# Optimization experiments

Hardware: AMD Instinct MI355X
Metric: run time of the kernel (lower is better)

The kernel has to match this reference:

```python
import jax, jax.numpy as jnp
import numpy as np

B, S, D, H = 2, 2048, 1024, 16
HD = D // H  # 64
ROPE_BASE = 10000.0


def setup_inputs() -> dict:
    key = jax.random.key(0)
    k1, k2, k3 = jax.random.split(key, 3)
    std = 1.0 / np.sqrt(D)
    x = jax.random.normal(k1, (B, S, D), dtype=jnp.float32)
    w_in = jax.random.normal(k2, (3 * D, D), dtype=jnp.float32) * std
    w_out = jax.random.normal(k3, (D, D), dtype=jnp.float32) * (std / np.sqrt(2.0))
    return {"x": x, "w_in": w_in, "w_out": w_out}


def _rope_cos_sin(seq_len, head_dim):
    inv_freq = 1.0 / (ROPE_BASE ** (jnp.arange(0, head_dim, 2, dtype=jnp.float32) / head_dim))
    t = jnp.arange(seq_len, dtype=jnp.float32)
    freqs = jnp.einsum("s,d->sd", t, inv_freq)          # [S, HD/2]
    emb = jnp.concatenate([freqs, freqs], axis=-1)       # [S, HD]
    return jnp.cos(emb)[None, :, None, :], jnp.sin(emb)[None, :, None, :]


def _rotate_half(x):
    x1, x2 = jnp.split(x, 2, axis=-1)
    return jnp.concatenate([-x2, x1], axis=-1)


def _apply_rope(x, cos, sin):
    return x * cos + _rotate_half(x) * sin


def reference(x, w_in, w_out):
    b, s, d = x.shape
    # fused QKV projection (no bias)
    qkv = x @ w_in.T                                      # [B, S, 3D]
    q, k, v = jnp.split(qkv, 3, axis=-1)
    q = q.reshape(b, s, H, HD)
    k = k.reshape(b, s, H, HD)
    v = v.reshape(b, s, H, HD)
    # rotary (offset = 0, no KV cache)
    cos, sin = _rope_cos_sin(s, HD)
    q = _apply_rope(q, cos, sin)
    k = _apply_rope(k, cos, sin)
    # causal SDPA, scale 1/sqrt(head_dim)
    scale = 1.0 / jnp.sqrt(jnp.asarray(HD, dtype=x.dtype))
    scores = jnp.einsum("bqhd,bkhd->bhqk", q, k) * scale  # [B, H, S, S]
    causal = jnp.tril(jnp.ones((s, s), dtype=bool))
    scores = jnp.where(causal, scores, jnp.asarray(-jnp.inf, dtype=scores.dtype))
    attn = jax.nn.softmax(scores, axis=-1)
    out = jnp.einsum("bhqk,bkhd->bqhd", attn, v).reshape(b, s, d)
    return out @ w_out.T
```

## Files before the change

kernel.cpp:

```cpp
#include <hip/hip_runtime.h>
#include <hip/hip_bf16.h>
#include <math.h>

#define NB 2
#define NS 2048
#define ND 1024
#define NH 16
#define HD 64
#define BS (NB*NS)
#define D3 (3*ND)
#define NT (NS/64)

typedef __bf16 bf16;
typedef __bf16 bf16x4 __attribute__((ext_vector_type(4)));
typedef __bf16 bf16x8 __attribute__((ext_vector_type(8)));
typedef float f32x4 __attribute__((ext_vector_type(4)));

#define MFMA16(a,b,c) __builtin_amdgcn_mfma_f32_16x16x32_bf16(a,b,c,0,0,0)

static __device__ inline f32x4 zero4() { f32x4 z; z[0]=0.f; z[1]=0.f; z[2]=0.f; z[3]=0.f; return z; }

__device__ __forceinline__ void gload_lds16(const bf16* g, bf16* l) {
    __builtin_amdgcn_global_load_lds(
        (__attribute__((address_space(1))) unsigned int*)g,
        (__attribute__((address_space(3))) unsigned int*)l, 16, 0, 0);
}

#define CVT1 (BS*ND/8)
#define CVT2 (D3*ND/8)
#define CVT3 (ND*ND/8)
#define CVTN (CVT1+CVT2+CVT3)
__global__ __launch_bounds__(256) void prep(
    const float* __restrict__ x, const float* __restrict__ w_in, const float* __restrict__ w_out,
    bf16* __restrict__ xb, bf16* __restrict__ winb, bf16* __restrict__ woutb,
    float2* __restrict__ csT)
{
    int i = blockIdx.x * 256 + threadIdx.x;
    if (i < CVTN) {
        const float* in; bf16* out; int j;
        if (i < CVT1)            { in = x;     out = xb;    j = i; }
        else if (i < CVT1+CVT2)  { in = w_in;  out = winb;  j = i - CVT1; }
        else                     { in = w_out; out = woutb; j = i - CVT1 - CVT2; }
        const float4* p = (const float4*)in;
        float4 a = p[j*2], b = p[j*2+1];
        bf16x8 o;
        o[0]=(bf16)a.x; o[1]=(bf16)a.y; o[2]=(bf16)a.z; o[3]=(bf16)a.w;
        o[4]=(bf16)b.x; o[5]=(bf16)b.y; o[6]=(bf16)b.z; o[7]=(bf16)b.w;
        ((bf16x8*)out)[j] = o;
    } else {
        int k = i - CVTN;
        int s = k >> 5, j = k & 31;
        float inv = __expf(-(float)j * (9.210340372f * 0.03125f));
        float ang = (float)s * inv;
        csT[k] = make_float2(cosf(ang), sinf(ang));
    }
}

__global__ __launch_bounds__(256, 2) void gemm_qkv(
    const bf16* __restrict__ A, const bf16* __restrict__ Bm,
    bf16* __restrict__ Qb, bf16* __restrict__ Kb, bf16* __restrict__ Vt,
    const float2* __restrict__ csT)
{
    __shared__ bf16 As[2][128*64];
    __shared__ bf16 Bs[2][192*64];
    int t = threadIdx.x;
    int lane = t & 63, w = t >> 6;
    int lr = lane & 15, lg = lane >> 4;
    int m0 = blockIdx.y * 128, n0 = blockIdx.x * 192;

    int srow8 = lane >> 3;
    int schunk = (lane & 7) ^ srow8;
    const bf16* gA = A  + (size_t)(m0 + srow8)*ND + schunk*8;
    const bf16* gB = Bm + (size_t)(n0 + srow8)*ND + schunk*8;

    auto stage = [&](int kt) {
        int buf = kt & 1, k0 = kt*64;
        #pragma unroll
        for (int i=0;i<4;i++) {
            int r0 = w*32 + i*8;
            gload_lds16(gA + (size_t)r0*ND + k0, &As[buf][r0*64]);
        }
        #pragma unroll
        for (int i=0;i<6;i++) {
            int r0 = w*48 + i*8;
            gload_lds16(gB + (size_t)r0*ND + k0, &Bs[buf][r0*64]);
        }
    };

    f32x4 acc[2][12];
    #pragma unroll
    for (int mm=0;mm<2;mm++)
        #pragma unroll
        for (int n=0;n<12;n++) acc[mm][n] = zero4();

    bf16x8 af[2][2], bfr[4][2];

    stage(0); stage(1);

    for (int kt = 0; kt < 16; kt++) {
        int cur = kt & 1;
        const bf16* as = &As[cur][0];
        const bf16* bs = &Bs[cur][0];
        if (kt < 15) asm volatile("s_waitcnt vmcnt(10)" ::: "memory");
        else         asm volatile("s_waitcnt vmcnt(0)" ::: "memory");
        __builtin_amdgcn_s_barrier();
        __builtin_amdgcn_sched_barrier(0);

        #pragma unroll
        for (int mm=0;mm<2;mm++) {
            int row = w*32 + mm*16 + lr;
            af[mm][0] = *(const bf16x8*)&as[row*64 + ((lg     ^ (row&7))*8)];
            af[mm][1] = *(const bf16x8*)&as[row*64 + (((4+lg) ^ (row&7))*8)];
        }

        #pragma unroll
        for (int g=0; g<3; g++) {
            #pragma unroll
            for (int nn=0;nn<4;nn++) {
                int row = g*64 + nn*16 + lr;
                bfr[nn][0] = *(const bf16x8*)&bs[row*64 + ((lg     ^ (row&7))*8)];
                bfr[nn][1] = *(const bf16x8*)&bs[row*64 + (((4+lg) ^ (row&7))*8)];
            }
            asm volatile("s_waitcnt lgkmcnt(0)" ::: "memory");
            __builtin_amdgcn_sched_barrier(0);
            if (g == 2) {
                __builtin_amdgcn_s_barrier();
                __builtin_amdgcn_sched_barrier(0);
                if (kt + 2 < 16) stage(kt + 2);
            }
            __builtin_amdgcn_s_setprio(1);
            #pragma unroll
            for (int ks=0;ks<2;ks++)
                #pragma unroll
                for (int mm=0;mm<2;mm++)
                    #pragma unroll
                    for (int nn=0;nn<4;nn++)
                        acc[mm][g*4+nn] = MFMA16(af[mm][ks], bfr[nn][ks], acc[mm][g*4+nn]);
            __builtin_amdgcn_s_setprio(0);
        }
    }

    const float qs = 0.125f * 1.44269504f;
    #pragma unroll
    for (int a=0;a<3;a++) {
        int colbase = n0 + a*64;
        int which = colbase >> 10;
        if (which == 2) {
            #pragma unroll
            for (int p=0;p<4;p++)
                #pragma unroll
                for (int mm=0;mm<2;mm++) {
                    int gcol = colbase + p*16 + lr;
                    int h = (gcol & 1023) >> 6, d = gcol & 63;
                    int grow = m0 + w*32 + mm*16 + lg*4;
                    int b = grow >> 11, s0 = grow & (NS-1);
                    int shi = s0 & ~63, j = s0 & 63;
                    int kp = ((j>>5)&1)*32 + ((j>>2)&3)*8 + ((j>>4)&1)*4;
                    bf16x4 pv;
                    #pragma unroll
                    for (int r=0;r<4;r++) pv[r] = (bf16)acc[mm][a*4+p][r];
                    *(bf16x4*)&Vt[((size_t)((b*NH + h)*HD + d))*NS + shi + kp] = pv;
                }
        } else {
            bf16* dst = (which == 0) ? Qb : Kb;
            #pragma unroll
            for (int p=0;p<2;p++)
                #pragma unroll
                for (int mm=0;mm<2;mm++) {
                    int gcol = colbase + p*16 + lr;
                    int h = (gcol & 1023) >> 6, j = gcol & 63;
                    int grow = m0 + w*32 + mm*16 + lg*4;
                    #pragma unroll
                    for (int r=0;r<4;r++) {
                        int gm = grow + r;
                        int b = gm >> 11, s = gm & (NS-1);
                        float2 cs = csT[(s<<5)+j];
                        float x1 = acc[mm][a*4+p][r], x2 = acc[mm][a*4+p+2][r];
                        float y1 = x1*cs.x - x2*cs.y;
                        float y2 = x2*cs.x + x1*cs.y;
                        if (which == 0) { y1 *= qs; y2 *= qs; }
                        size_t off = ((size_t)((b*NH + h)*NS + s))*HD;
                        dst[off + j]      = (bf16)y1;
                        dst[off + j + 32] = (bf16)y2;
                    }
                }
        }
    }
}

__global__ __launch_bounds__(256) void gemm_out(
    const bf16* __restrict__ A, const bf16* __restrict__ Bm,
    float* __restrict__ C, int M, int N, int K)
{
    __shared__ bf16 As[2][128*64];
    __shared__ bf16 Bs[2][128*64];
    int t = threadIdx.x;
    int lane = t & 63, w = t >> 6;
    int wr = w >> 1, wc = w & 1;
    int lr = lane & 15, lg = lane >> 4;
    int m0 = blockIdx.y * 128, n0 = blockIdx.x * 128;

    int srow = lane >> 3;
    int schunk = (lane & 7) ^ srow;
    const bf16* gA = &A [(size_t)(m0 + w*32 + srow)*K + schunk*8];
    const bf16* gB = &Bm[(size_t)(n0 + w*32 + srow)*K + schunk*8];

    auto stage = [&](int kt) {
        int buf = kt & 1;
        bf16* lA = &As[buf][w*2048];
        bf16* lB = &Bs[buf][w*2048];
        int k0 = kt * 64;
        #pragma unroll
        for (int i=0;i<4;i++) {
            gload_lds16(gA + (size_t)(i*8)*K + k0, lA + i*512);
            gload_lds16(gB + (size_t)(i*8)*K + k0, lB + i*512);
        }
    };

    f32x4 acc[4][4];
    for (int m=0;m<4;m++) for (int n=0;n<4;n++) acc[m][n] = zero4();

    int nt = K >> 6;
    stage(0);
    stage(1);

    for (int kt = 0; kt < nt; kt++) {
        int cur = kt & 1;
        if (kt < nt-1) asm volatile("s_waitcnt vmcnt(8)" ::: "memory");
        else           asm volatile("s_waitcnt vmcnt(0)" ::: "memory");
        __builtin_amdgcn_s_barrier();
        __builtin_amdgcn_sched_barrier(0);

        bf16x8 af[2][4], bfr[2][4];
        #pragma unroll
        for (int ks=0;ks<2;ks++) {
            #pragma unroll
            for (int m=0;m<4;m++) {
                int row = wr*64 + m*16 + lr;
                af[ks][m] = *(const bf16x8*)&As[cur][row*64 + (((ks*4+lg) ^ (row&7))*8)];
            }
            #pragma unroll
            for (int n=0;n<4;n++) {
                int row = wc*64 + n*16 + lr;
                bfr[ks][n] = *(const bf16x8*)&Bs[cur][row*64 + (((ks*4+lg) ^ (row&7))*8)];
            }
        }
        asm volatile("s_waitcnt lgkmcnt(0)" ::: "memory");
        __builtin_amdgcn_sched_barrier(0);
        __builtin_amdgcn_s_barrier();
        __builtin_amdgcn_sched_barrier(0);

        if (kt + 2 < nt) stage(kt + 2);

        __builtin_amdgcn_s_setprio(1);
        #pragma unroll
        for (int ks=0;ks<2;ks++)
            #pragma unroll
            for (int m=0;m<4;m++)
                #pragma unroll
                for (int n=0;n<4;n++)
                    acc[m][n] = MFMA16(af[ks][m], bfr[ks][n], acc[m][n]);
        __builtin_amdgcn_s_setprio(0);
    }

    for (int m=0;m<4;m++) for (int n=0;n<4;n++) {
        int grow = m0 + wr*64 + m*16 + lg*4;
        int gcol = n0 + wc*64 + n*16 + lr;
        for (int r=0;r<4;r++)
            C[(size_t)(grow+r) * N + gcol] = acc[m][n][r];
    }
}

__global__ __launch_bounds__(256, 4) void attn_fwd(
    const bf16* __restrict__ Qb, const bf16* __restrict__ Kb, const bf16* __restrict__ Vp,
    bf16* __restrict__ AO)
{
    __shared__ bf16 Ks[2][64*64];
    __shared__ bf16 Vs[2][64*64];
    int t = threadIdx.x;
    int lane = t & 63, w = t >> 6;
    int lr = lane & 15, lg = lane >> 4;
    int wgid = blockIdx.x;
    int g = wgid >> 5;
    int qt = (g < 8) ? 31 - g : (g < 16) ? g - 8 : (g < 24) ? 39 - g : g - 16;
    int bh = wgid & 31;
    int b = bh >> 4, h = bh & 15;
    size_t base = (size_t)bh * NS * HD;
    int q0 = qt*64 + w*16;

    bf16x8 qf[2];
    #pragma unroll
    for (int c=0;c<2;c++)
        qf[c] = *(const bf16x8*)&Qb[base + (size_t)(q0+lr)*HD + c*32 + lg*8];

    bf16x8 onesf;
    #pragma unroll
    for (int i=0;i<8;i++) onesf[i] = (bf16)1.0f;

    f32x4 o[4];
    f32x4 lacc = zero4();
    #pragma unroll
    for (int n=0;n<4;n++) o[n] = zero4();
    f32x4 minit;
    minit[0] = -12.f; minit[1] = -12.f; minit[2] = -12.f; minit[3] = -12.f;

    int srow8 = lane >> 3;
    int schunk = (lane & 7) ^ srow8;
    int srcrow = w*8 + srow8;
    const bf16* gK = Kb + base + (size_t)srcrow*HD + schunk*8;
    const bf16* gV = Vp + base + (size_t)srcrow*NS + schunk*8;

    auto stage = [&](int kt) {
        int buf = kt & 1;
        int kv0 = kt * 64;
        #pragma unroll
        for (int i=0;i<2;i++) {
            gload_lds16(gK + (size_t)(kv0 + i*32)*HD, &Ks[buf][(i*32 + w*8)*64]);
            gload_lds16(gV + (size_t)(i*32)*NS + kv0, &Vs[buf][(i*32 + w*8)*64]);
        }
    };

    stage(0);
    if (qt > 0) stage(1);

    for (int kt = 0; kt <= qt; kt++) {
        int cur = kt & 1;
        bool last = (kt == qt);
        if (!last) asm volatile("s_waitcnt vmcnt(4)" ::: "memory");
        else       asm volatile("s_waitcnt vmcnt(0)" ::: "memory");
        __builtin_amdgcn_s_barrier();
        __builtin_amdgcn_sched_barrier(0);

        const bf16* ksb = &Ks[cur][0];
        const bf16* vsb = &Vs[cur][0];

        bf16x8 kf[4][2], vf[2][4];
        #pragma unroll
        for (int kb=0;kb<4;kb++) {
            int row = kb*16 + lr;
            kf[kb][0] = *(const bf16x8*)&ksb[row*64 + ((lg     ^ (row&7))*8)];
            kf[kb][1] = *(const bf16x8*)&ksb[row*64 + (((4+lg) ^ (row&7))*8)];
        }
        #pragma unroll
        for (int c=0;c<2;c++)
            #pragma unroll
            for (int n=0;n<4;n++) {
                int row = n*16 + lr;
                vf[c][n] = *(const bf16x8*)&vsb[row*64 + (((c*4+lg) ^ (row&7))*8)];
            }

        f32x4 sc[4];
        __builtin_amdgcn_s_setprio(1);
        #pragma unroll
        for (int kb=0;kb<4;kb++) {
            sc[kb] = MFMA16(kf[kb][0], qf[0], minit);
            sc[kb] = MFMA16(kf[kb][1], qf[1], sc[kb]);
        }
        __builtin_amdgcn_s_setprio(0);

        if (last) {
            int qi = q0 + lr;
            #pragma unroll
            for (int kb=0;kb<4;kb++)
                #pragma unroll
                for (int rr=0;rr<4;rr++)
                    if (kt*64 + kb*16 + lg*4 + rr > qi) sc[kb][rr] = -__builtin_inff();
        }

        bf16x8 pa[2];
        #pragma unroll
        for (int c=0;c<2;c++) {
            bf16x8 v;
            #pragma unroll
            for (int i=0;i<8;i++) v[i] = (bf16)exp2f(sc[c*2 + (i>>2)][i&3]);
            pa[c] = v;
        }

        asm volatile("s_waitcnt lgkmcnt(0)" ::: "memory");
        __builtin_amdgcn_sched_barrier(0);
        __builtin_amdgcn_s_barrier();
        __builtin_amdgcn_sched_barrier(0);

        if (kt + 2 <= qt) stage(kt + 2);

        __builtin_amdgcn_s_setprio(1);
        #pragma unroll
        for (int c=0;c<2;c++) {
            lacc = MFMA16(onesf, pa[c], lacc);
            #pragma unroll
            for (int n=0;n<4;n++)
                o[n] = MFMA16(vf[c][n], pa[c], o[n]);
        }
        __builtin_amdgcn_s_setprio(0);
    }

    float inv = 1.0f / lacc[0];
    int q = q0 + lr;
    #pragma unroll
    for (int n=0;n<4;n++) {
        bf16x4 ov;
        #pragma unroll
        for (int rr=0;rr<4;rr++) ov[rr] = (bf16)(o[n][rr] * inv);
        *(bf16x4*)&AO[((size_t)(b*NS + q)*NH + h)*HD + n*16 + lg*4] = ov;
    }
}

extern "C" void kernel_launch(void* const* d_in, const int* in_sizes, int n_in,
                              void* d_out, int out_size, void* d_ws, size_t ws_size,
                              hipStream_t stream) {
    const float* x     = (const float*)d_in[0];
    const float* w_in  = (const float*)d_in[1];
    const float* w_out = (const float*)d_in[2];
    float* out = (float*)d_out;

    char* p = (char*)d_ws;
    bf16* xb    = (bf16*)p; p += (size_t)BS*ND*2;
    bf16* winb  = (bf16*)p; p += (size_t)D3*ND*2;
    bf16* woutb = (bf16*)p; p += (size_t)ND*ND*2;
    bf16* Qb    = (bf16*)p; p += (size_t)NB*NH*NS*HD*2;
    bf16* Kb    = (bf16*)p; p += (size_t)NB*NH*NS*HD*2;
    bf16* Vp    = (bf16*)p; p += (size_t)NB*NH*NS*HD*2;
    bf16* AO    = (bf16*)p; p += (size_t)BS*ND*2;
    float2* csT = (float2*)p; p += (size_t)NS*32*8;

    prep<<<(CVTN + NS*32)/256, 256, 0, stream>>>(x, w_in, w_out, xb, winb, woutb, csT);
    gemm_qkv<<<dim3(D3/192, BS/128), 256, 0, stream>>>(xb, winb, Qb, Kb, Vp, csT);
    attn_fwd<<<NB*NH*NT, 256, 0, stream>>>(Qb, Kb, Vp, AO);
    gemm_out<<<dim3(ND/128, BS/128), 256, 0, stream>>>(AO, woutb, out, BS, ND, ND);
}
```

Measured before the change: 91.50 us.

## Rewrite attention with 32x32x16 MFMA and 128-row query tiles

The attention kernel now uses 32x32x16 bf16 MFMAs. Each workgroup covers 128 query rows (32 per wave) instead of 64, which halves the grid and shares each staged K/V tile across more queries. The P-matrix operand layout is rebuilt with cross-half-wave shuffles, and the V transpose layout in the QKV GEMM epilogue is simplified to match. Waves skip fully masked key tiles. In exchange, register pressure rises (occupancy hint lowered to 2), shuffles are added, the grid has fewer blocks, and waves in the same block do uneven amounts of work.

```diff
diff --git a/kernel.cpp b/kernel.cpp
--- a/kernel.cpp
+++ b/kernel.cpp
@@ -15,8 +15,11 @@
 typedef __bf16 bf16x4 __attribute__((ext_vector_type(4)));
 typedef __bf16 bf16x8 __attribute__((ext_vector_type(8)));
 typedef float f32x4 __attribute__((ext_vector_type(4)));
+typedef float f32x16 __attribute__((ext_vector_type(16)));
+typedef unsigned int u32;
 
 #define MFMA16(a,b,c) __builtin_amdgcn_mfma_f32_16x16x32_bf16(a,b,c,0,0,0)
+#define MFMA32(a,b,c) __builtin_amdgcn_mfma_f32_32x32x16_bf16(a,b,c,0,0,0)
 
 static __device__ inline f32x4 zero4() { f32x4 z; z[0]=0.f; z[1]=0.f; z[2]=0.f; z[3]=0.f; return z; }
 
@@ -154,12 +157,10 @@
                     int h = (gcol & 1023) >> 6, d = gcol & 63;
                     int grow = m0 + w*32 + mm*16 + lg*4;
                     int b = grow >> 11, s0 = grow & (NS-1);
-                    int shi = s0 & ~63, j = s0 & 63;
-                    int kp = ((j>>5)&1)*32 + ((j>>2)&3)*8 + ((j>>4)&1)*4;
                     bf16x4 pv;
                     #pragma unroll
                     for (int r=0;r<4;r++) pv[r] = (bf16)acc[mm][a*4+p][r];
-                    *(bf16x4*)&Vt[((size_t)((b*NH + h)*HD + d))*NS + shi + kp] = pv;
+                    *(bf16x4*)&Vt[((size_t)((b*NH + h)*HD + d))*NS + s0] = pv;
                 }
         } else {
             bf16* dst = (which == 0) ? Qb : Kb;
@@ -271,7 +272,7 @@
     }
 }
 
-__global__ __launch_bounds__(256, 4) void attn_fwd(
+__global__ __launch_bounds__(256, 2) void attn_fwd(
     const bf16* __restrict__ Qb, const bf16* __restrict__ Kb, const bf16* __restrict__ Vp,
     bf16* __restrict__ AO)
 {
@@ -279,30 +280,29 @@
     __shared__ bf16 Vs[2][64*64];
     int t = threadIdx.x;
     int lane = t & 63, w = t >> 6;
-    int lr = lane & 15, lg = lane >> 4;
+    int lq = lane & 31, hh = lane >> 5;
     int wgid = blockIdx.x;
     int g = wgid >> 5;
-    int qt = (g < 8) ? 31 - g : (g < 16) ? g - 8 : (g < 24) ? 39 - g : g - 16;
+    int qt2 = (g < 8) ? 15 - g : g - 8;
     int bh = wgid & 31;
     int b = bh >> 4, h = bh & 15;
     size_t base = (size_t)bh * NS * HD;
-    int q0 = qt*64 + w*16;
-
-    bf16x8 qf[2];
-    #pragma unroll
-    for (int c=0;c<2;c++)
-        qf[c] = *(const bf16x8*)&Qb[base + (size_t)(q0+lr)*HD + c*32 + lg*8];
+    int q0w = qt2*128 + w*32;
+    int q = q0w + lq;
+    int nvis = 2*qt2 + 2;
+
+    bf16x8 qf[4];
+    #pragma unroll
+    for (int tt=0;tt<4;tt++)
+        qf[tt] = *(const bf16x8*)&Qb[base + (size_t)q*HD + tt*16 + hh*8];
 
     bf16x8 onesf;
     #pragma unroll
     for (int i=0;i<8;i++) onesf[i] = (bf16)1.0f;
 
-    f32x4 o[4];
-    f32x4 lacc = zero4();
-    #pragma unroll
-    for (int n=0;n<4;n++) o[n] = zero4();
-    f32x4 minit;
-    minit[0] = -12.f; minit[1] = -12.f; minit[2] = -12.f; minit[3] = -12.f;
+    f32x16 o[2], lacc, minit;
+    #pragma unroll
+    for (int i=0;i<16;i++) { o[0][i]=0.f; o[1][i]=0.f; lacc[i]=0.f; minit[i]=-12.f; }
 
     int srow8 = lane >> 3;
     int schunk = (lane & 7) ^ srow8;
@@ -321,88 +321,119 @@
     };
 
     stage(0);
-    if (qt > 0) stage(1);
-
-    for (int kt = 0; kt <= qt; kt++) {
+    if (nvis > 1) stage(1);
+
+    for (int kt = 0; kt < nvis; kt++) {
         int cur = kt & 1;
-        bool last = (kt == qt);
+        int kv0 = kt*64;
+        bool last = (kt + 1 == nvis);
         if (!last) asm volatile("s_waitcnt vmcnt(4)" ::: "memory");
         else       asm volatile("s_waitcnt vmcnt(0)" ::: "memory");
         __builtin_amdgcn_s_barrier();
         __builtin_amdgcn_sched_barrier(0);
 
+        bool active = (kv0 <= q0w + 31);
         const bf16* ksb = &Ks[cur][0];
         const bf16* vsb = &Vs[cur][0];
-
-        bf16x8 kf[4][2], vf[2][4];
-        #pragma unroll
-        for (int kb=0;kb<4;kb++) {
-            int row = kb*16 + lr;
-            kf[kb][0] = *(const bf16x8*)&ksb[row*64 + ((lg     ^ (row&7))*8)];
-            kf[kb][1] = *(const bf16x8*)&ksb[row*64 + (((4+lg) ^ (row&7))*8)];
-        }
-        #pragma unroll
-        for (int c=0;c<2;c++)
-            #pragma unroll
-            for (int n=0;n<4;n++) {
-                int row = n*16 + lr;
-                vf[c][n] = *(const bf16x8*)&vsb[row*64 + (((c*4+lg) ^ (row&7))*8)];
-            }
-
-        f32x4 sc[4];
-        __builtin_amdgcn_s_setprio(1);
-        #pragma unroll
-        for (int kb=0;kb<4;kb++) {
-            sc[kb] = MFMA16(kf[kb][0], qf[0], minit);
-            sc[kb] = MFMA16(kf[kb][1], qf[1], sc[kb]);
-        }
-        __builtin_amdgcn_s_setprio(0);
-
-        if (last) {
-            int qi = q0 + lr;
-            #pragma unroll
-            for (int kb=0;kb<4;kb++)
-                #pragma unroll
-                for (int rr=0;rr<4;rr++)
-                    if (kt*64 + kb*16 + lg*4 + rr > qi) sc[kb][rr] = -__builtin_inff();
-        }
-
-        bf16x8 pa[2];
-        #pragma unroll
-        for (int c=0;c<2;c++) {
-            bf16x8 v;
-            #pragma unroll
-            for (int i=0;i<8;i++) v[i] = (bf16)exp2f(sc[c*2 + (i>>2)][i&3]);
-            pa[c] = v;
+        bf16x8 vf[2][4];
+        bf16x8 pa[4];
+
+        if (active) {
+            bf16x8 kf[2][4];
+            #pragma unroll
+            for (int kb=0;kb<2;kb++)
+                #pragma unroll
+                for (int tt=0;tt<4;tt++) {
+                    int row = kb*32 + lq;
+                    kf[kb][tt] = *(const bf16x8*)&ksb[row*64 + (((tt*2+hh) ^ (row&7))*8)];
+                }
+
+            f32x16 sc[2];
+            __builtin_amdgcn_s_setprio(1);
+            #pragma unroll
+            for (int kb=0;kb<2;kb++) {
+                sc[kb] = minit;
+                #pragma unroll
+                for (int tt=0;tt<4;tt++)
+                    sc[kb] = MFMA32(kf[kb][tt], qf[tt], sc[kb]);
+            }
+            __builtin_amdgcn_s_setprio(0);
+
+            #pragma unroll
+            for (int db=0;db<2;db++)
+                #pragma unroll
+                for (int tt=0;tt<4;tt++) {
+                    int row = db*32 + lq;
+                    vf[db][tt] = *(const bf16x8*)&vsb[row*64 + (((tt*2+hh) ^ (row&7))*8)];
+                }
+
+            if (kv0 + 63 > q0w) {
+                #pragma unroll
+                for (int kb=0;kb<2;kb++)
+                    #pragma unroll
+                    for (int r=0;r<16;r++) {
+                        int key = kv0 + kb*32 + (r&3) + 8*(r>>2) + 4*hh;
+                        if (key > q) sc[kb][r] = -__builtin_inff();
+                    }
+            }
+
+            #pragma unroll
+            for (int s=0;s<4;s++) {
+                int kb = s >> 1, bb = 8*(s&1);
+                bf16x4 qA, qB;
+                #pragma unroll
+                for (int j=0;j<4;j++) {
+                    qA[j] = (bf16)exp2f(sc[kb][bb+j]);
+                    qB[j] = (bf16)exp2f(sc[kb][bb+4+j]);
+                }
+                union { bf16x4 v; u32 u[2]; } cA, cB, cS, cL, cH;
+                cA.v = qA; cB.v = qB;
+                u32 s0_ = hh ? cA.u[0] : cB.u[0];
+                u32 s1_ = hh ? cA.u[1] : cB.u[1];
+                u32 r0 = (u32)__shfl_xor((int)s0_, 32);
+                u32 r1 = (u32)__shfl_xor((int)s1_, 32);
+                cL.u[0] = hh ? r0 : cA.u[0];
+                cL.u[1] = hh ? r1 : cA.u[1];
+                cH.u[0] = hh ? cB.u[0] : r0;
+                cH.u[1] = hh ? cB.u[1] : r1;
+                bf16x8 v;
+                #pragma unroll
+                for (int j=0;j<4;j++) { v[j] = cL.v[j]; v[4+j] = cH.v[j]; }
+                pa[s] = v;
+            }
         }
 
         asm volatile("s_waitcnt lgkmcnt(0)" ::: "memory");
         __builtin_amdgcn_sched_barrier(0);
         __builtin_amdgcn_s_barrier();
         __builtin_amdgcn_sched_barrier(0);
-
-        if (kt + 2 <= qt) stage(kt + 2);
-
-        __builtin_amdgcn_s_setprio(1);
-        #pragma unroll
-        for (int c=0;c<2;c++) {
-            lacc = MFMA16(onesf, pa[c], lacc);
-            #pragma unroll
-            for (int n=0;n<4;n++)
-                o[n] = MFMA16(vf[c][n], pa[c], o[n]);
-        }
-        __builtin_amdgcn_s_setprio(0);
+        if (kt + 2 < nvis) stage(kt + 2);
+
+        if (active) {
+            __builtin_amdgcn_s_setprio(1);
+            #pragma unroll
+            for (int tt=0;tt<4;tt++)
+                lacc = MFMA32(onesf, pa[tt], lacc);
+            #pragma unroll
+            for (int db=0;db<2;db++)
+                #pragma unroll
+                for (int tt=0;tt<4;tt++)
+                    o[db] = MFMA32(vf[db][tt], pa[tt], o[db]);
+            __builtin_amdgcn_s_setprio(0);
+        }
     }
 
     float inv = 1.0f / lacc[0];
-    int q = q0 + lr;
-    #pragma unroll
-    for (int n=0;n<4;n++) {
-        bf16x4 ov;
-        #pragma unroll
-        for (int rr=0;rr<4;rr++) ov[rr] = (bf16)(o[n][rr] * inv);
-        *(bf16x4*)&AO[((size_t)(b*NS + q)*NH + h)*HD + n*16 + lg*4] = ov;
-    }
+    #pragma unroll
+    for (int db=0;db<2;db++)
+        #pragma unroll
+        for (int rg=0;rg<4;rg++) {
+            int d0 = db*32 + rg*8 + hh*4;
+            bf16x4 ov;
+            #pragma unroll
+            for (int rr=0;rr<4;rr++) ov[rr] = (bf16)(o[db][rg*4+rr] * inv);
+            *(bf16x4*)&AO[((size_t)(b*NS + q)*NH + h)*HD + d0] = ov;
+        }
 }
 
 extern "C" void kernel_launch(void* const* d_in, const int* in_sizes, int n_in,
@@ -425,6 +456,6 @@
 
     prep<<<(CVTN + NS*32)/256, 256, 0, stream>>>(x, w_in, w_out, xb, winb, woutb, csT);
     gemm_qkv<<<dim3(D3/192, BS/128), 256, 0, stream>>>(xb, winb, Qb, Kb, Vp, csT);
-    attn_fwd<<<NB*NH*NT, 256, 0, stream>>>(Qb, Kb, Vp, AO);
+    attn_fwd<<<NB*NH*16, 256, 0, stream>>>(Qb, Kb, Vp, AO);
     gemm_out<<<dim3(ND/128, BS/128), 256, 0, stream>>>(AO, woutb, out, BS, ND, ND);
 }
```

Measured after the change: 108.3 us. 18.4% more time.
